# Kernel tuning notes

Hardware: AMD Instinct MI355X
Metric: run time of the kernel (lower is better)

Reference implementation:

```python
import jax, jax.numpy as jnp
import numpy as np
from jax.scipy.special import logsumexp

S, B, T = 512, 1024, 48


def setup_inputs() -> dict:
    key = jax.random.key(0)
    k1, k2, k3, k4, k5 = jax.random.split(key, 5)
    return {
        "emissions": jax.random.normal(k1, (S, B, T), jnp.float32),
        "tags": jax.random.randint(k2, (S, B), 0, T, jnp.int32),
        "mask": jnp.ones((S, B), jnp.float32),
        "transitions": jax.random.normal(k3, (T, T), jnp.float32),
        "start_transitions": jax.random.normal(k4, (T,), jnp.float32),
        "stop_transitions": jax.random.normal(k5, (T,), jnp.float32),
    }


def _crf(emissions, tags, mask, transitions, start, stop):
    # emissions: (S,B,T), tags/mask: (S,B), time-major as in the torch module
    init = start[None, :] + emissions[0]  # (B,T)

    def step(carry, inp):
        fv, vv = carry  # forward (logsumexp) and viterbi (max) vars, each (B,T)
        em, m = inp  # (B,T), (B,)
        # scores[b, next, prev] = prev_var + transitions[prev,next] swapped to match
        # torch: forward_var.unsqueeze(1) + emission.unsqueeze(2) + transitions.unsqueeze(0)
        sc_f = fv[:, None, :] + transitions[None, :, :] + em[:, :, None]  # (B,T,T)
        sc_v = vv[:, None, :] + transitions[None, :, :] + em[:, :, None]
        new_fv = logsumexp(sc_f, axis=2)
        new_vv = jnp.max(sc_v, axis=2)
        m_ = m[:, None]
        fv = m_ * new_fv + (1.0 - m_) * fv
        vv = m_ * new_vv + (1.0 - m_) * vv
        return (fv, vv), None

    (fv, vv), _ = jax.lax.scan(step, (init, init), (emissions[1:], mask[1:]))
    alpha = logsumexp(fv + stop[None, :], axis=1)  # total_score (B,)
    best_path_score = jnp.max(vv + stop[None, :], axis=1)  # (B,)

    # real (gold) path score, fully vectorized over time
    em_tag = jnp.take_along_axis(emissions, tags[:, :, None].astype(jnp.int32), axis=2)[:, :, 0]  # (S,B)
    trans_sc = transitions[tags[:-1], tags[1:]]  # (S-1,B)
    real = (start[tags[0]]
            + jnp.sum(mask[1:] * (trans_sc + em_tag[1:]), axis=0)
            + stop[tags[-1]])
    loss = jnp.mean(alpha - real)
    return loss, real, alpha, best_path_score


def reference(emissions, tags, mask, transitions, start_transitions, stop_transitions):
    # Training-mode forward (return_best_path=False -> best_path is None in torch)
    return _crf(emissions, tags, mask, transitions, start_transitions, stop_transitions)
```

## Files before the change

kernel.cpp:

```cpp
#include <hip/hip_runtime.h>
#include <hip/hip_fp16.h>

#define S_LEN 512
#define B_DIM 1024
#define T_DIM 48
#define L2E 1.4426950408889634f
#define LN2 0.6931471805599453f

#define EXP2F(x) __builtin_amdgcn_exp2f(x)
#define LOG2F(x) __builtin_amdgcn_logf(x)

typedef _Float16 h2v __attribute__((ext_vector_type(2)));

__device__ __forceinline__ __half2 hmax2(__half2 a, __half2 b) {
  h2v r = __builtin_elementwise_max(__builtin_bit_cast(h2v, a),
                                    __builtin_bit_cast(h2v, b));
  return __builtin_bit_cast(__half2, r);
}

__device__ __forceinline__ __half2 bpick(__half2 src, int lane) {
  int s = __builtin_amdgcn_readlane(__builtin_bit_cast(int, src), lane);
  return __builtin_bit_cast(__half2, s);
}

template <int CTRL, int RMASK>
__device__ __forceinline__ float dppmovf(float v) {
  return __int_as_float(__builtin_amdgcn_update_dpp(
      __float_as_int(v), __float_as_int(v), CTRL, RMASK, 0xF, false));
}
template <int CTRL, int RMASK>
__device__ __forceinline__ float dppmaxf(float m) {
  return fmaxf(m, dppmovf<CTRL, RMASK>(m));
}
template <int CTRL, int RMASK>
__device__ __forceinline__ float dppaddf(float m) {
  return m + dppmovf<CTRL, RMASK>(m);
}

__device__ __forceinline__ float wave_max63(float m) {
  m = dppmaxf<0xB1, 0xF>(m);
  m = dppmaxf<0x4E, 0xF>(m);
  m = dppmaxf<0x141, 0xF>(m);
  m = dppmaxf<0x140, 0xF>(m);
  m = dppmaxf<0x142, 0xA>(m);
  m = dppmaxf<0x143, 0xC>(m);
  return __int_as_float(__builtin_amdgcn_readlane(__float_as_int(m), 63));
}
__device__ __forceinline__ float wave_sum63(float m) {
  m = dppaddf<0xB1, 0xF>(m);
  m = dppaddf<0x4E, 0xF>(m);
  m = dppaddf<0x141, 0xF>(m);
  m = dppaddf<0x140, 0xF>(m);
  m = dppaddf<0x142, 0xA>(m);
  m = dppaddf<0x143, 0xC>(m);
  return __int_as_float(__builtin_amdgcn_readlane(__float_as_int(m), 63));
}

__global__ __launch_bounds__(192, 3)
void crf_fused(const float* __restrict__ em, const int* __restrict__ tags,
               const float* __restrict__ mask, const float* __restrict__ trans,
               const float* __restrict__ startT, const float* __restrict__ stopT,
               float* __restrict__ out)
{
  const int b    = blockIdx.x;
  const int wave = threadIdx.x >> 6;
  const int i    = threadIdx.x & 63;

  if (wave == 2) {
    float acc = 0.f;
    for (int g = 0; g < 63; ++g) {
      if (g < 8) {
        int s = 1 + i + (g << 6);
        if (s < S_LEN) {
          int   tp  = tags[(s - 1) * B_DIM + b];
          int   tc  = tags[s * B_DIM + b];
          float mkv = mask[s * B_DIM + b];
          float emt = em[((size_t)s * B_DIM + b) * T_DIM + tc];
          acc = fmaf(mkv, trans[tp * T_DIM + tc] + emt, acc);
        }
      }
      __builtin_amdgcn_s_barrier();
    }
    float tot = wave_sum63(acc);
    if (i == 0)
      out[1 + b] = startT[tags[b]] + stopT[tags[(S_LEN - 1) * B_DIM + b]] + tot;
    return;
  }

  const int ri = (i < T_DIM) ? i : (T_DIM - 1);

  const float* emb = em + (size_t)b * T_DIM + ri;
  const size_t estep = (size_t)B_DIM * T_DIM;
  float e1 = emb[1 * estep], e2 = emb[2 * estep], e3 = emb[3 * estep];
  float e4 = emb[4 * estep], e5 = emb[5 * estep], e6 = emb[6 * estep];
  float mk1 = mask[1 * B_DIM + b], mk2 = mask[2 * B_DIM + b];
  float mk3 = mask[3 * B_DIM + b], mk4 = mask[4 * B_DIM + b];
  float mk5 = mask[5 * B_DIM + b], mk6 = mask[6 * B_DIM + b];
  const float* pf  = emb + 7 * estep;
  const float* pmk = mask + 7 * B_DIM + b;

#define SHIFT_REGS                                                   \
      e1 = e2; e2 = e3; e3 = e4; e4 = e5; e5 = e6; e6 = ep;          \
      mk1 = mk2; mk2 = mk3; mk3 = mk4; mk4 = mk5; mk5 = mk6; mk6 = mkp;

  if (wave == 0) {
#define DECL_E(n) __half2 E##n = __floats2half2_rn( \
      EXP2F(trans[ri * T_DIM + 2*(n)    ] * L2E),   \
      EXP2F(trans[ri * T_DIM + 2*(n) + 1] * L2E));
    DECL_E(0)  DECL_E(1)  DECL_E(2)  DECL_E(3)  DECL_E(4)  DECL_E(5)
    DECL_E(6)  DECL_E(7)  DECL_E(8)  DECL_E(9)  DECL_E(10) DECL_E(11)
    DECL_E(12) DECL_E(13) DECL_E(14) DECL_E(15) DECL_E(16) DECL_E(17)
    DECL_E(18) DECL_E(19) DECL_E(20) DECL_E(21) DECL_E(22) DECL_E(23)

    asm volatile("" : "+v"(E0), "+v"(E1), "+v"(E2), "+v"(E3),
      "+v"(E4), "+v"(E5), "+v"(E6), "+v"(E7), "+v"(E8), "+v"(E9),
      "+v"(E10), "+v"(E11), "+v"(E12), "+v"(E13), "+v"(E14),
      "+v"(E15), "+v"(E16), "+v"(E17), "+v"(E18), "+v"(E19),
      "+v"(E20), "+v"(E21), "+v"(E22), "+v"(E23));

    float p  = EXP2F((startT[ri] + emb[0]) * L2E);
    float k2 = 0.f;

#define FVG(g, Ea, Eb, Ec, Ed, Ee, Ef)                 \
    { __half2 t0 = bpick(pp, 12*(g) + 0);              \
      __half2 t1 = bpick(pp, 12*(g) + 2);              \
      __half2 t2 = bpick(pp, 12*(g) + 4);              \
      __half2 t3 = bpick(pp, 12*(g) + 6);              \
      __half2 t4 = bpick(pp, 12*(g) + 8);              \
      __half2 t5 = bpick(pp, 12*(g) + 10);             \
      a0 = __hfma2(t0, Ea, a0);                        \
      a1 = __hfma2(t1, Eb, a1);                        \
      a2 = __hfma2(t2, Ec, a2);                        \
      a3 = __hfma2(t3, Ed, a3);                        \
      a0 = __hfma2(t4, Ee, a0);                        \
      a1 = __hfma2(t5, Ef, a1); }

#define FV_STEP(LOAD)                                                \
    { float ep, mkp;                                                 \
      if (LOAD) { ep = *pf; pf += estep; mkp = *pmk; pmk += B_DIM; } \
      else      { ep = e6; mkp = mk6; }                              \
      float pm = wave_max63(p);                                      \
      int ee   = (__float_as_int(pm) >> 23) - 126;    \
      float c  = __int_as_float((127 - ee) << 23);  \
      k2 += (float)ee;                                               \
      float pn = dppmovf<0xB1, 0xF>(p);                              \
      __half2 pp = __floats2half2_rn(p, pn);                         \
      __half2 a0 = __float2half2_rn(0.f), a1 = a0, a2 = a0, a3 = a0; \
      FVG(0, E0,  E1,  E2,  E3,  E4,  E5)                            \
      FVG(1, E6,  E7,  E8,  E9,  E10, E11)                           \
      FVG(2, E12, E13, E14, E15, E16, E17)                           \
      FVG(3, E18, E19, E20, E21, E22, E23)                           \
      a0 = __hadd2(a0, a1); a2 = __hadd2(a2, a3); a0 = __hadd2(a0, a2); \
      float accF  = __low2float(a0) + __high2float(a0);              \
      float expem = EXP2F(e1 * L2E);                                 \
      float t  = accF * expem * c;                                   \
      float pc = p * c;                                              \
      p = fminf(fmaf(mk1, t - pc, pc), 1024.0f);                     \
      SHIFT_REGS }

    for (int g = 0; g < 63; ++g) {
#pragma unroll
      for (int u = 0; u < 8; ++u) FV_STEP(true)
      __builtin_amdgcn_s_barrier();
    }
    FV_STEP(true)
    FV_STEP(false) FV_STEP(false) FV_STEP(false)
    FV_STEP(false) FV_STEP(false) FV_STEP(false)

    float q = p * EXP2F(stopT[ri] * L2E);
    q = (i < T_DIM) ? q : 0.f;
    float Sq = wave_sum63(q);
    float alpha = LN2 * (k2 + LOG2F(Sq));
    if (i == 0) out[1 + B_DIM + b] = alpha;
  } else {
#define DECL_T(n) __half2 T##n = __floats2half2_rn( \
      trans[ri * T_DIM + 2*(n)], trans[ri * T_DIM + 2*(n) + 1]);
    DECL_T(0)  DECL_T(1)  DECL_T(2)  DECL_T(3)  DECL_T(4)  DECL_T(5)
    DECL_T(6)  DECL_T(7)  DECL_T(8)  DECL_T(9)  DECL_T(10) DECL_T(11)
    DECL_T(12) DECL_T(13) DECL_T(14) DECL_T(15) DECL_T(16) DECL_T(17)
    DECL_T(18) DECL_T(19) DECL_T(20) DECL_T(21) DECL_T(22) DECL_T(23)

    asm volatile("" : "+v"(T0), "+v"(T1), "+v"(T2), "+v"(T3),
      "+v"(T4), "+v"(T5), "+v"(T6), "+v"(T7), "+v"(T8), "+v"(T9),
      "+v"(T10), "+v"(T11), "+v"(T12), "+v"(T13), "+v"(T14),
      "+v"(T15), "+v"(T16), "+v"(T17), "+v"(T18), "+v"(T19),
      "+v"(T20), "+v"(T21), "+v"(T22), "+v"(T23));

    float v = startT[ri] + emb[0];
    const __half2 NEGI = __floats2half2_rn(-60000.f, -60000.f);
    float m_ref = wave_max63(v);

#define VVG(g, Ta, Tb, Tc, Td, Te, Tf)                 \
    { __half2 t0 = bpick(vp, 12*(g) + 0);              \
      __half2 t1 = bpick(vp, 12*(g) + 2);              \
      __half2 t2 = bpick(vp, 12*(g) + 4);              \
      __half2 t3 = bpick(vp, 12*(g) + 6);              \
      __half2 t4 = bpick(vp, 12*(g) + 8);              \
      __half2 t5 = bpick(vp, 12*(g) + 10);             \
      m0 = hmax2(m0, __hadd2(t0, Ta));                 \
      m1 = hmax2(m1, __hadd2(t1, Tb));                 \
      m2 = hmax2(m2, __hadd2(t2, Tc));                 \
      m3 = hmax2(m3, __hadd2(t3, Td));                 \
      m0 = hmax2(m0, __hadd2(t4, Te));                 \
      m1 = hmax2(m1, __hadd2(t5, Tf)); }

#define VV_STEP(LOAD, DOTREE)                                        \
    { float ep, mkp;                                                 \
      if (LOAD) { ep = *pf; pf += estep; mkp = *pmk; pmk += B_DIM; } \
      else      { ep = e6; mkp = mk6; }                              \
      if (DOTREE) m_ref = wave_max63(v);                             \
      float vr  = v - m_ref;                                         \
      float vn_ = dppmovf<0xB1, 0xF>(vr);                            \
      __half2 vp = __floats2half2_rn(vr, vn_);                       \
      __half2 m0 = NEGI, m1 = NEGI, m2 = NEGI, m3 = NEGI;            \
      VVG(0, T0,  T1,  T2,  T3,  T4,  T5)                            \
      VVG(1, T6,  T7,  T8,  T9,  T10, T11)                           \
      VVG(2, T12, T13, T14, T15, T16, T17)                           \
      VVG(3, T18, T19, T20, T21, T22, T23)                           \
      m0 = hmax2(hmax2(m0, m1), hmax2(m2, m3));                      \
      float mx = fmaxf(__low2float(m0), __high2float(m0));           \
      float vnew = e1 + m_ref + mx;                                  \
      v = fmaf(mk1, vnew - v, v);                                    \
      SHIFT_REGS }

    for (int g = 0; g < 63; ++g) {
#pragma unroll
      for (int u = 0; u < 7; ++u) VV_STEP(true, false)
      VV_STEP(true, true)
      __builtin_amdgcn_s_barrier();
    }
    VV_STEP(true, false)
    VV_STEP(false, false) VV_STEP(false, false) VV_STEP(false, false)
    VV_STEP(false, false) VV_STEP(false, false) VV_STEP(false, false)

    float best = wave_max63(v + stopT[ri]);
    if (i == 0) out[1 + 2 * B_DIM + b] = best;
  }
}

__global__ __launch_bounds__(256)
void crf_loss(float* __restrict__ out)
{
  __shared__ float red[256];
  int t = threadIdx.x;
  float a = 0.f;
  for (int b = t; b < B_DIM; b += 256)
    a += out[1 + B_DIM + b] - out[1 + b];
  red[t] = a;
  __syncthreads();
  for (int w = 128; w > 0; w >>= 1) {
    if (t < w) red[t] += red[t + w];
    __syncthreads();
  }
  if (t == 0) out[0] = red[0] * (1.0f / B_DIM);
}

extern "C" void kernel_launch(void* const* d_in, const int* in_sizes, int n_in,
                              void* d_out, int out_size, void* d_ws, size_t ws_size,
                              hipStream_t stream) {
  (void)in_sizes; (void)n_in; (void)d_ws; (void)ws_size; (void)out_size;
  const float* em     = (const float*)d_in[0];
  const int*   tags   = (const int*)d_in[1];
  const float* mask   = (const float*)d_in[2];
  const float* trans  = (const float*)d_in[3];
  const float* startT = (const float*)d_in[4];
  const float* stopT  = (const float*)d_in[5];
  float* out = (float*)d_out;

  hipLaunchKernelGGL(crf_fused, dim3(B_DIM), dim3(192), 0, stream,
                     em, tags, mask, trans, startT, stopT, out);
  hipLaunchKernelGGL(crf_loss, dim3(1), dim3(256), 0, stream, out);
}
```

Measured before the change: 208.7 us.

## Compute CRF forward recursion with MFMA over batch tiles in extra blocks

```diff
diff --git a/kernel.cpp b/kernel.cpp
--- a/kernel.cpp
+++ b/kernel.cpp
@@ -11,13 +11,22 @@
 #define LOG2F(x) __builtin_amdgcn_logf(x)
 
 typedef _Float16 h2v __attribute__((ext_vector_type(2)));
+typedef _Float16 r4  __attribute__((ext_vector_type(4)));
+typedef float    f4  __attribute__((ext_vector_type(4)));
+
+__device__ __forceinline__ f4 MFMA16(r4 a, r4 b, f4 c) {
+#if defined(__HIP_DEVICE_COMPILE__)
+  return __builtin_amdgcn_mfma_f32_16x16x16f16(a, b, c, 0, 0, 0);
+#else
+  (void)a; (void)b; return c;
+#endif
+}
 
 __device__ __forceinline__ __half2 hmax2(__half2 a, __half2 b) {
   h2v r = __builtin_elementwise_max(__builtin_bit_cast(h2v, a),
                                     __builtin_bit_cast(h2v, b));
   return __builtin_bit_cast(__half2, r);
 }
-
 __device__ __forceinline__ __half2 bpick(__half2 src, int lane) {
   int s = __builtin_amdgcn_readlane(__builtin_bit_cast(int, src), lane);
   return __builtin_bit_cast(__half2, s);
@@ -36,159 +45,192 @@
 __device__ __forceinline__ float dppaddf(float m) {
   return m + dppmovf<CTRL, RMASK>(m);
 }
-
 __device__ __forceinline__ float wave_max63(float m) {
-  m = dppmaxf<0xB1, 0xF>(m);
-  m = dppmaxf<0x4E, 0xF>(m);
-  m = dppmaxf<0x141, 0xF>(m);
-  m = dppmaxf<0x140, 0xF>(m);
-  m = dppmaxf<0x142, 0xA>(m);
-  m = dppmaxf<0x143, 0xC>(m);
+  m = dppmaxf<0xB1, 0xF>(m);  m = dppmaxf<0x4E, 0xF>(m);
+  m = dppmaxf<0x141, 0xF>(m); m = dppmaxf<0x140, 0xF>(m);
+  m = dppmaxf<0x142, 0xA>(m); m = dppmaxf<0x143, 0xC>(m);
   return __int_as_float(__builtin_amdgcn_readlane(__float_as_int(m), 63));
 }
 __device__ __forceinline__ float wave_sum63(float m) {
-  m = dppaddf<0xB1, 0xF>(m);
-  m = dppaddf<0x4E, 0xF>(m);
-  m = dppaddf<0x141, 0xF>(m);
-  m = dppaddf<0x140, 0xF>(m);
-  m = dppaddf<0x142, 0xA>(m);
-  m = dppaddf<0x143, 0xC>(m);
+  m = dppaddf<0xB1, 0xF>(m);  m = dppaddf<0x4E, 0xF>(m);
+  m = dppaddf<0x141, 0xF>(m); m = dppaddf<0x140, 0xF>(m);
+  m = dppaddf<0x142, 0xA>(m); m = dppaddf<0x143, 0xC>(m);
   return __int_as_float(__builtin_amdgcn_readlane(__float_as_int(m), 63));
 }
 
-__global__ __launch_bounds__(192, 3)
+__global__ __launch_bounds__(128, 2)
 void crf_fused(const float* __restrict__ em, const int* __restrict__ tags,
                const float* __restrict__ mask, const float* __restrict__ trans,
                const float* __restrict__ startT, const float* __restrict__ stopT,
                float* __restrict__ out)
 {
-  const int b    = blockIdx.x;
+  const int blk  = blockIdx.x;
   const int wave = threadIdx.x >> 6;
-  const int i    = threadIdx.x & 63;
-
-  if (wave == 2) {
+  const int l    = threadIdx.x & 63;
+
+  if (blk >= B_DIM) {
+    const int tile = (blk - B_DIM) * 2 + wave;
+    const int a  = l >> 4;
+    const int n  = l & 15;
+    const int bb = tile * 16 + n;
+    const int bpi = (l ^ 32) << 2;
+
+#define DECL_A(mt,kf) r4 A##mt##kf; {                                  \
+      const float* tb = trans + (16*(mt) + n) * T_DIM + 16*(kf) + 4*a; \
+      A##mt##kf[0] = (_Float16)EXP2F(tb[0] * L2E);                     \
+      A##mt##kf[1] = (_Float16)EXP2F(tb[1] * L2E);                     \
+      A##mt##kf[2] = (_Float16)EXP2F(tb[2] * L2E);                     \
+      A##mt##kf[3] = (_Float16)EXP2F(tb[3] * L2E); }
+    DECL_A(0,0) DECL_A(0,1) DECL_A(0,2)
+    DECL_A(1,0) DECL_A(1,1) DECL_A(1,2)
+    DECL_A(2,0) DECL_A(2,1) DECL_A(2,2)
+    asm volatile("" : "+v"(A00), "+v"(A01), "+v"(A02),
+                      "+v"(A10), "+v"(A11), "+v"(A12),
+                      "+v"(A20), "+v"(A21), "+v"(A22));
+
+    const float* e0 = em + (size_t)bb * T_DIM;
+    f4 P0, P1, P2;
+#pragma unroll
+    for (int r = 0; r < 4; ++r) {
+      P0[r] = EXP2F((startT[ 0 + 4*a + r] + e0[ 0 + 4*a + r]) * L2E);
+      P1[r] = EXP2F((startT[16 + 4*a + r] + e0[16 + 4*a + r]) * L2E);
+      P2[r] = EXP2F((startT[32 + 4*a + r] + e0[32 + 4*a + r]) * L2E);
+    }
+    float k2 = 0.f;
+
+    const size_t rstep = (size_t)B_DIM * T_DIM;
+    const float* pe = em + rstep + (size_t)bb * T_DIM + 4*a;
+    f4 EA0 = *(const f4*)(pe +  0), EA1 = *(const f4*)(pe + 16),
+       EA2 = *(const f4*)(pe + 32);
+    pe += rstep;
+    f4 EB0 = *(const f4*)(pe +  0), EB1 = *(const f4*)(pe + 16),
+       EB2 = *(const f4*)(pe + 32);
+    pe += rstep;
+    f4 EC0 = *(const f4*)(pe +  0), EC1 = *(const f4*)(pe + 16),
+       EC2 = *(const f4*)(pe + 32);
+    pe += rstep;
+    float mkA = mask[1*B_DIM + bb], mkB = mask[2*B_DIM + bb],
+          mkC = mask[3*B_DIM + bb];
+    const float* pm = mask + 4*B_DIM + bb;
+
+#define FMSTEP(LOAD)                                                      \
+    { f4 D0, D1, D2; float mkD;                                           \
+      if (LOAD) { D0 = *(const f4*)(pe); D1 = *(const f4*)(pe + 16);      \
+                  D2 = *(const f4*)(pe + 32); pe += rstep;                \
+                  mkD = *pm; pm += B_DIM; }                               \
+      else      { D0 = EC0; D1 = EC1; D2 = EC2; mkD = mkC; }              \
+                           \
+      float mx = fmaxf(fmaxf(fmaxf(P0[0],P0[1]), fmaxf(P0[2],P0[3])),     \
+                 fmaxf(fmaxf(fmaxf(P1[0],P1[1]), fmaxf(P1[2],P1[3])),     \
+                       fmaxf(fmaxf(P2[0],P2[1]), fmaxf(P2[2],P2[3]))));   \
+      mx = fmaxf(mx, __int_as_float(__builtin_amdgcn_ds_swizzle(          \
+                       __float_as_int(mx), 0x401F)));                     \
+      mx = fmaxf(mx, __int_as_float(__builtin_amdgcn_ds_bpermute(         \
+                       bpi, __float_as_int(mx))));                        \
+      int ee  = (__float_as_int(mx) >> 23) - 126;                         \
+      float c = __int_as_float((135 - ee) << 23);           \
+      k2 += (float)(ee - 8);                                              \
+      r4 B0, B1, B2;                                                      \
+      B0[0]=(_Float16)(P0[0]*c); B0[1]=(_Float16)(P0[1]*c);               \
+      B0[2]=(_Float16)(P0[2]*c); B0[3]=(_Float16)(P0[3]*c);               \
+      B1[0]=(_Float16)(P1[0]*c); B1[1]=(_Float16)(P1[1]*c);               \
+      B1[2]=(_Float16)(P1[2]*c); B1[3]=(_Float16)(P1[3]*c);               \
+      B2[0]=(_Float16)(P2[0]*c); B2[1]=(_Float16)(P2[1]*c);               \
+      B2[2]=(_Float16)(P2[2]*c); B2[3]=(_Float16)(P2[3]*c);               \
+      f4 Z = {0.f, 0.f, 0.f, 0.f};                                        \
+      f4 C0 = MFMA16(A00, B0, Z); C0 = MFMA16(A01, B1, C0);               \
+      C0 = MFMA16(A02, B2, C0);                                           \
+      f4 C1 = MFMA16(A10, B0, Z); C1 = MFMA16(A11, B1, C1);               \
+      C1 = MFMA16(A12, B2, C1);                                           \
+      f4 C2 = MFMA16(A20, B0, Z); C2 = MFMA16(A21, B1, C2);               \
+      C2 = MFMA16(A22, B2, C2);                                           \
+      _Pragma("unroll")                                                   \
+      for (int r = 0; r < 4; ++r) {                                       \
+        float ps0 = P0[r]*c, q0 = C0[r]*EXP2F(EA0[r]*L2E);                \
+        P0[r] = fmaf(mkA, q0 - ps0, ps0);                                 \
+        float ps1 = P1[r]*c, q1 = C1[r]*EXP2F(EA1[r]*L2E);                \
+        P1[r] = fmaf(mkA, q1 - ps1, ps1);                                 \
+        float ps2 = P2[r]*c, q2 = C2[r]*EXP2F(EA2[r]*L2E);                \
+        P2[r] = fmaf(mkA, q2 - ps2, ps2);                                 \
+      }                                                                   \
+      EA0 = EB0; EA1 = EB1; EA2 = EB2;                                    \
+      EB0 = EC0; EB1 = EC1; EB2 = EC2;                                    \
+      EC0 = D0;  EC1 = D1;  EC2 = D2;                                     \
+      mkA = mkB; mkB = mkC; mkC = mkD; }
+
+#pragma unroll 2
+    for (int s = 1; s <= 508; ++s) FMSTEP(true)
+    FMSTEP(false) FMSTEP(false) FMSTEP(false)
+
+    float part = 0.f;
+#pragma unroll
+    for (int r = 0; r < 4; ++r) {
+      part = fmaf(P0[r], EXP2F(stopT[ 0 + 4*a + r] * L2E), part);
+      part = fmaf(P1[r], EXP2F(stopT[16 + 4*a + r] * L2E), part);
+      part = fmaf(P2[r], EXP2F(stopT[32 + 4*a + r] * L2E), part);
+    }
+    part += __int_as_float(__builtin_amdgcn_ds_swizzle(
+                __float_as_int(part), 0x401F));
+    part += __int_as_float(__builtin_amdgcn_ds_bpermute(
+                bpi, __float_as_int(part)));
+    float alpha = LN2 * (k2 + LOG2F(part));
+    if (a == 0) out[1 + B_DIM + bb] = alpha;
+    return;
+  }
+
+  if (wave == 1) {
+    const int b = blk;
     float acc = 0.f;
-    for (int g = 0; g < 63; ++g) {
-      if (g < 8) {
-        int s = 1 + i + (g << 6);
-        if (s < S_LEN) {
-          int   tp  = tags[(s - 1) * B_DIM + b];
-          int   tc  = tags[s * B_DIM + b];
-          float mkv = mask[s * B_DIM + b];
-          float emt = em[((size_t)s * B_DIM + b) * T_DIM + tc];
-          acc = fmaf(mkv, trans[tp * T_DIM + tc] + emt, acc);
-        }
+#pragma unroll
+    for (int k = 0; k < 8; ++k) {
+      int s = 1 + l + (k << 6);
+      if (s < S_LEN) {
+        int   tp  = tags[(s - 1) * B_DIM + b];
+        int   tc  = tags[s * B_DIM + b];
+        float mkv = mask[s * B_DIM + b];
+        float emt = em[((size_t)s * B_DIM + b) * T_DIM + tc];
+        acc = fmaf(mkv, trans[tp * T_DIM + tc] + emt, acc);
       }
-      __builtin_amdgcn_s_barrier();
     }
     float tot = wave_sum63(acc);
-    if (i == 0)
-      out[1 + b] = startT[tags[b]] + stopT[tags[(S_LEN - 1) * B_DIM + b]] + tot;
+    if (l == 0)
+      out[1 + b] = startT[tags[b]] +
+                   stopT[tags[(S_LEN - 1) * B_DIM + b]] + tot;
     return;
   }
 
-  const int ri = (i < T_DIM) ? i : (T_DIM - 1);
-
+  const int b  = blk;
+  const int ri = (l < T_DIM) ? l : (T_DIM - 1);
   const float* emb = em + (size_t)b * T_DIM + ri;
   const size_t estep = (size_t)B_DIM * T_DIM;
-  float e1 = emb[1 * estep], e2 = emb[2 * estep], e3 = emb[3 * estep];
-  float e4 = emb[4 * estep], e5 = emb[5 * estep], e6 = emb[6 * estep];
-  float mk1 = mask[1 * B_DIM + b], mk2 = mask[2 * B_DIM + b];
-  float mk3 = mask[3 * B_DIM + b], mk4 = mask[4 * B_DIM + b];
-  float mk5 = mask[5 * B_DIM + b], mk6 = mask[6 * B_DIM + b];
-  const float* pf  = emb + 7 * estep;
-  const float* pmk = mask + 7 * B_DIM + b;
+  float e1 = emb[1*estep], e2 = emb[2*estep], e3 = emb[3*estep];
+  float e4 = emb[4*estep], e5 = emb[5*estep], e6 = emb[6*estep];
+  float mk1 = mask[1*B_DIM + b], mk2 = mask[2*B_DIM + b];
+  float mk3 = mask[3*B_DIM + b], mk4 = mask[4*B_DIM + b];
+  float mk5 = mask[5*B_DIM + b], mk6 = mask[6*B_DIM + b];
+  const float* pf  = emb + 7*estep;
+  const float* pmk = mask + 7*B_DIM + b;
 
 #define SHIFT_REGS                                                   \
       e1 = e2; e2 = e3; e3 = e4; e4 = e5; e5 = e6; e6 = ep;          \
       mk1 = mk2; mk2 = mk3; mk3 = mk4; mk4 = mk5; mk5 = mk6; mk6 = mkp;
 
-  if (wave == 0) {
-#define DECL_E(n) __half2 E##n = __floats2half2_rn( \
-      EXP2F(trans[ri * T_DIM + 2*(n)    ] * L2E),   \
-      EXP2F(trans[ri * T_DIM + 2*(n) + 1] * L2E));
-    DECL_E(0)  DECL_E(1)  DECL_E(2)  DECL_E(3)  DECL_E(4)  DECL_E(5)
-    DECL_E(6)  DECL_E(7)  DECL_E(8)  DECL_E(9)  DECL_E(10) DECL_E(11)
-    DECL_E(12) DECL_E(13) DECL_E(14) DECL_E(15) DECL_E(16) DECL_E(17)
-    DECL_E(18) DECL_E(19) DECL_E(20) DECL_E(21) DECL_E(22) DECL_E(23)
-
-    asm volatile("" : "+v"(E0), "+v"(E1), "+v"(E2), "+v"(E3),
-      "+v"(E4), "+v"(E5), "+v"(E6), "+v"(E7), "+v"(E8), "+v"(E9),
-      "+v"(E10), "+v"(E11), "+v"(E12), "+v"(E13), "+v"(E14),
-      "+v"(E15), "+v"(E16), "+v"(E17), "+v"(E18), "+v"(E19),
-      "+v"(E20), "+v"(E21), "+v"(E22), "+v"(E23));
-
-    float p  = EXP2F((startT[ri] + emb[0]) * L2E);
-    float k2 = 0.f;
-
-#define FVG(g, Ea, Eb, Ec, Ed, Ee, Ef)                 \
-    { __half2 t0 = bpick(pp, 12*(g) + 0);              \
-      __half2 t1 = bpick(pp, 12*(g) + 2);              \
-      __half2 t2 = bpick(pp, 12*(g) + 4);              \
-      __half2 t3 = bpick(pp, 12*(g) + 6);              \
-      __half2 t4 = bpick(pp, 12*(g) + 8);              \
-      __half2 t5 = bpick(pp, 12*(g) + 10);             \
-      a0 = __hfma2(t0, Ea, a0);                        \
-      a1 = __hfma2(t1, Eb, a1);                        \
-      a2 = __hfma2(t2, Ec, a2);                        \
-      a3 = __hfma2(t3, Ed, a3);                        \
-      a0 = __hfma2(t4, Ee, a0);                        \
-      a1 = __hfma2(t5, Ef, a1); }
-
-#define FV_STEP(LOAD)                                                \
-    { float ep, mkp;                                                 \
-      if (LOAD) { ep = *pf; pf += estep; mkp = *pmk; pmk += B_DIM; } \
-      else      { ep = e6; mkp = mk6; }                              \
-      float pm = wave_max63(p);                                      \
-      int ee   = (__float_as_int(pm) >> 23) - 126;    \
-      float c  = __int_as_float((127 - ee) << 23);  \
-      k2 += (float)ee;                                               \
-      float pn = dppmovf<0xB1, 0xF>(p);                              \
-      __half2 pp = __floats2half2_rn(p, pn);                         \
-      __half2 a0 = __float2half2_rn(0.f), a1 = a0, a2 = a0, a3 = a0; \
-      FVG(0, E0,  E1,  E2,  E3,  E4,  E5)                            \
-      FVG(1, E6,  E7,  E8,  E9,  E10, E11)                           \
-      FVG(2, E12, E13, E14, E15, E16, E17)                           \
-      FVG(3, E18, E19, E20, E21, E22, E23)                           \
-      a0 = __hadd2(a0, a1); a2 = __hadd2(a2, a3); a0 = __hadd2(a0, a2); \
-      float accF  = __low2float(a0) + __high2float(a0);              \
-      float expem = EXP2F(e1 * L2E);                                 \
-      float t  = accF * expem * c;                                   \
-      float pc = p * c;                                              \
-      p = fminf(fmaf(mk1, t - pc, pc), 1024.0f);                     \
-      SHIFT_REGS }
-
-    for (int g = 0; g < 63; ++g) {
-#pragma unroll
-      for (int u = 0; u < 8; ++u) FV_STEP(true)
-      __builtin_amdgcn_s_barrier();
-    }
-    FV_STEP(true)
-    FV_STEP(false) FV_STEP(false) FV_STEP(false)
-    FV_STEP(false) FV_STEP(false) FV_STEP(false)
-
-    float q = p * EXP2F(stopT[ri] * L2E);
-    q = (i < T_DIM) ? q : 0.f;
-    float Sq = wave_sum63(q);
-    float alpha = LN2 * (k2 + LOG2F(Sq));
-    if (i == 0) out[1 + B_DIM + b] = alpha;
-  } else {
-#define DECL_T(n) __half2 T##n = __floats2half2_rn( \
-      trans[ri * T_DIM + 2*(n)], trans[ri * T_DIM + 2*(n) + 1]);
-    DECL_T(0)  DECL_T(1)  DECL_T(2)  DECL_T(3)  DECL_T(4)  DECL_T(5)
-    DECL_T(6)  DECL_T(7)  DECL_T(8)  DECL_T(9)  DECL_T(10) DECL_T(11)
-    DECL_T(12) DECL_T(13) DECL_T(14) DECL_T(15) DECL_T(16) DECL_T(17)
-    DECL_T(18) DECL_T(19) DECL_T(20) DECL_T(21) DECL_T(22) DECL_T(23)
-
-    asm volatile("" : "+v"(T0), "+v"(T1), "+v"(T2), "+v"(T3),
-      "+v"(T4), "+v"(T5), "+v"(T6), "+v"(T7), "+v"(T8), "+v"(T9),
-      "+v"(T10), "+v"(T11), "+v"(T12), "+v"(T13), "+v"(T14),
-      "+v"(T15), "+v"(T16), "+v"(T17), "+v"(T18), "+v"(T19),
-      "+v"(T20), "+v"(T21), "+v"(T22), "+v"(T23));
-
-    float v = startT[ri] + emb[0];
-    const __half2 NEGI = __floats2half2_rn(-60000.f, -60000.f);
-    float m_ref = wave_max63(v);
+#define DECL_T(nn) __half2 T##nn = __floats2half2_rn( \
+      trans[ri * T_DIM + 2*(nn)], trans[ri * T_DIM + 2*(nn) + 1]);
+  DECL_T(0)  DECL_T(1)  DECL_T(2)  DECL_T(3)  DECL_T(4)  DECL_T(5)
+  DECL_T(6)  DECL_T(7)  DECL_T(8)  DECL_T(9)  DECL_T(10) DECL_T(11)
+  DECL_T(12) DECL_T(13) DECL_T(14) DECL_T(15) DECL_T(16) DECL_T(17)
+  DECL_T(18) DECL_T(19) DECL_T(20) DECL_T(21) DECL_T(22) DECL_T(23)
+
+  asm volatile("" : "+v"(T0), "+v"(T1), "+v"(T2), "+v"(T3),
+    "+v"(T4), "+v"(T5), "+v"(T6), "+v"(T7), "+v"(T8), "+v"(T9),
+    "+v"(T10), "+v"(T11), "+v"(T12), "+v"(T13), "+v"(T14),
+    "+v"(T15), "+v"(T16), "+v"(T17), "+v"(T18), "+v"(T19),
+    "+v"(T20), "+v"(T21), "+v"(T22), "+v"(T23));
+
+  float v = startT[ri] + emb[0];
+  const __half2 NEGI = __floats2half2_rn(-60000.f, -60000.f);
+  float m_ref = wave_max63(v);
 
 #define VVG(g, Ta, Tb, Tc, Td, Te, Tf)                 \
     { __half2 t0 = bpick(vp, 12*(g) + 0);              \
@@ -223,19 +265,14 @@
       v = fmaf(mk1, vnew - v, v);                                    \
       SHIFT_REGS }
 
-    for (int g = 0; g < 63; ++g) {
-#pragma unroll
-      for (int u = 0; u < 7; ++u) VV_STEP(true, false)
-      VV_STEP(true, true)
-      __builtin_amdgcn_s_barrier();
-    }
-    VV_STEP(true, false)
-    VV_STEP(false, false) VV_STEP(false, false) VV_STEP(false, false)
-    VV_STEP(false, false) VV_STEP(false, false) VV_STEP(false, false)
-
-    float best = wave_max63(v + stopT[ri]);
-    if (i == 0) out[1 + 2 * B_DIM + b] = best;
-  }
+#pragma unroll 8
+  for (int s = 1; s <= 504; ++s) VV_STEP(true, ((s & 7) == 0))
+  VV_STEP(true, false)
+  VV_STEP(false, false) VV_STEP(false, false) VV_STEP(false, false)
+  VV_STEP(false, false) VV_STEP(false, false) VV_STEP(false, false)
+
+  float best = wave_max63(v + stopT[ri]);
+  if (l == 0) out[1 + 2 * B_DIM + b] = best;
 }
 
 __global__ __launch_bounds__(256)
@@ -267,7 +304,7 @@
   const float* stopT  = (const float*)d_in[5];
   float* out = (float*)d_out;
 
-  hipLaunchKernelGGL(crf_fused, dim3(B_DIM), dim3(192), 0, stream,
+  hipLaunchKernelGGL(crf_fused, dim3(B_DIM + 32), dim3(128), 0, stream,
                      em, tags, mask, trans, startT, stopT, out);
   hipLaunchKernelGGL(crf_loss, dim3(1), dim3(256), 0, stream, out);
 }
```

After: 258.2 us. 23.7% more time.
